# Kernel optimization log

Hardware: AMD Instinct MI355X
Metric: run time of the kernel (lower is better)

The kernel has to match this reference:

```python
import jax, jax.numpy as jnp
import numpy as np

B, S, HID = 2, 2048, 2048
H, K, D = 32, 8, 64          # query heads, kv heads, head_dim
G = H // K                   # GQA group size
ROPE_MSCALE = 1.2            # constant rope_mscale applied to q and k
SM_SCALE = 1.0 / (D ** 0.5)  # flash_attn default softmax scale


def rotate_half(x):
    h = x.shape[-1] // 2
    return jnp.concatenate([-x[..., h:], x[..., :h]], axis=-1)


def setup_inputs() -> dict:
    key = jax.random.key(0)
    k1, k2, k3, k4 = jax.random.split(key, 4)
    hidden_states = jax.random.normal(k1, (B, S, HID), dtype=jnp.float32)
    # standard rotary tables: cos/sin of shape [S, D]
    inv_freq = 1.0 / (10000.0 ** (jnp.arange(0, D, 2, dtype=jnp.float32) / D))
    freqs = jnp.outer(jnp.arange(S, dtype=jnp.float32), inv_freq)  # [S, D/2]
    emb = jnp.concatenate([freqs, freqs], axis=-1)                 # [S, D]
    cos, sin = jnp.cos(emb), jnp.sin(emb)
    per_head_scale = 1.0 + 0.1 * jax.random.normal(k2, (B, H), dtype=jnp.float32)
    Wqkv = jax.random.normal(k3, ((H + 2 * K) * D, HID), dtype=jnp.float32) * (HID ** -0.5)
    Wo = jax.random.normal(k4, (HID, H * D), dtype=jnp.float32) * ((H * D) ** -0.5)
    return {"cos": cos, "sin": sin, "hidden_states": hidden_states,
            "per_head_scale": per_head_scale, "Wqkv": Wqkv, "Wo": Wo}


def reference(cos, sin, hidden_states, per_head_scale, Wqkv, Wo):
    # fused QKV projection (CastedLinear, no bias)
    qkv = jnp.einsum('bsh,oh->bso', hidden_states, Wqkv)          # [B,S,(H+2K)*D]
    qkv = qkv.reshape(B, S, H + 2 * K, D)
    q = qkv[:, :, :H]                 # [B,S,H,D]
    k = qkv[:, :, H:H + K]            # [B,S,K,D]
    v = qkv[:, :, H + K:]             # [B,S,K,D]
    # rotary embedding: cos/sin [S,D] -> broadcast over heads via [S,1,D]
    c = cos[:, None, :]
    s_ = sin[:, None, :]
    q = q * c + rotate_half(q) * s_
    k = k * c + rotate_half(k) * s_
    # rope_mscale
    q = q * ROPE_MSCALE
    k = k * ROPE_MSCALE
    # per-head scale on queries: [B,H] -> [B,1,H,1]
    q = q * per_head_scale[:, None, :, None]
    # GQA attention without materializing repeated K/V: group query heads
    qg = q.reshape(B, S, K, G, D)
    scores = jnp.einsum('bqkgd,bskd->bkgqs', qg, k) * SM_SCALE    # [B,K,G,Sq,Sk]
    causal = jnp.arange(S)[:, None] >= jnp.arange(S)[None, :]     # [Sq,Sk]
    scores = jnp.where(causal, scores, jnp.finfo(scores.dtype).min)
    probs = jax.nn.softmax(scores, axis=-1)
    out = jnp.einsum('bkgqs,bskd->bqkgd', probs, v).reshape(B, S, H * D)
    return jnp.einsum('bso,ho->bsh', out, Wo)                     # o_proj
```

## Files before the change

### kernel.cpp

```cpp
#include <hip/hip_runtime.h>
#include <stdint.h>

typedef unsigned short u16;
typedef short short8 __attribute__((ext_vector_type(8)));
typedef float f32x4 __attribute__((ext_vector_type(4)));
typedef uint32_t u32x4 __attribute__((ext_vector_type(4)));

#define S_LEN 2048
#define NQH 32
#define NKH 8
#define DHD 64

__device__ __forceinline__ float b2f(u16 u){
  union { uint32_t i; float f; } c; c.i = ((uint32_t)u) << 16; return c.f;
}
__device__ __forceinline__ u16 f2b(float f){
  union { float f; uint32_t i; } c; c.f = f;
  uint32_t r = c.i + 0x7fffu + ((c.i >> 16) & 1u);
  return (u16)(r >> 16);
}
__device__ __forceinline__ uint32_t cvt_pk_bf16(float lo, float hi){
  uint32_t r;
  asm("v_cvt_pk_bf16_f32 %0, %1, %2" : "=v"(r) : "v"(lo), "v"(hi));
  return r;
}
__device__ __forceinline__ void gload_lds16(const void* g, void* l){
  __builtin_amdgcn_global_load_lds((const __attribute__((address_space(1))) uint32_t*)g,
                                   (__attribute__((address_space(3))) uint32_t*)l, 16, 0, 0);
}

__global__ __launch_bounds__(256) void cvt_all(const float* __restrict__ hs,
                                               const float* __restrict__ wq,
                                               const float* __restrict__ wo,
                                               u16* __restrict__ hsB,
                                               u16* __restrict__ wqB,
                                               u16* __restrict__ woB){
  int i = blockIdx.x * 256 + threadIdx.x;
  const float* src; u16* dst; int off;
  if (i < 2097152)      { src = hs; dst = hsB; off = i; }
  else if (i < 3670016) { src = wq; dst = wqB; off = i - 2097152; }
  else                  { src = wo; dst = woB; off = i - 3670016; }
  float4 v = ((const float4*)src)[off];
  uint2 o;
  o.x = (uint32_t)f2b(v.x) | ((uint32_t)f2b(v.y) << 16);
  o.y = (uint32_t)f2b(v.z) | ((uint32_t)f2b(v.w) << 16);
  ((uint2*)dst)[off] = o;
}

template<int OUT_F32>
__global__ __launch_bounds__(256)
void gemm_bt(const u16* __restrict__ A, const u16* __restrict__ Bm,
             void* __restrict__ Cp, int N, int K)
{
  __shared__ alignas(16) u16 lA[128 * 64];
  __shared__ alignas(16) u16 lB[128 * 64];
  const int tid = threadIdx.x;
  const int w = tid >> 6, l = tid & 63;
  const int lg = l >> 4, lc = l & 15;
  const int wm = w >> 1, wn = w & 1;
  const int m0 = blockIdx.y * 128, n0 = blockIdx.x * 128;
  const int srow = l >> 3, sc = l & 7;
  const size_t ldb = (size_t)K * 2;
  f32x4 acc[4][4] = {};
  const int kiters = K >> 6;
  for (int kt = 0; kt < kiters; ++kt){
    __syncthreads();
#pragma unroll
    for (int i = 0; i < 4; ++i){
      const int row = (i * 4 + w) * 8 + srow;
      const int gc = ((sc ^ (row & 7)) << 4);
      gload_lds16((const char*)A + (size_t)(m0 + row) * ldb + (size_t)kt * 128 + gc,
                  (char*)lA + row * 128 + sc * 16);
    }
#pragma unroll
    for (int i = 0; i < 4; ++i){
      const int row = (i * 4 + w) * 8 + srow;
      const int gc = ((sc ^ (row & 7)) << 4);
      gload_lds16((const char*)Bm + (size_t)(n0 + row) * ldb + (size_t)kt * 128 + gc,
                  (char*)lB + row * 128 + sc * 16);
    }
    __syncthreads();
#pragma unroll
    for (int kk = 0; kk < 2; ++kk){
      short8 af[4], bfr[4];
#pragma unroll
      for (int mi = 0; mi < 4; ++mi){
        const int row = wm * 64 + mi * 16 + lc;
        const int cc = (kk * 4 + lg) ^ (row & 7);
        af[mi] = *(const short8*)((const char*)lA + row * 128 + cc * 16);
      }
#pragma unroll
      for (int ni = 0; ni < 4; ++ni){
        const int row = wn * 64 + ni * 16 + lc;
        const int cc = (kk * 4 + lg) ^ (row & 7);
        bfr[ni] = *(const short8*)((const char*)lB + row * 128 + cc * 16);
      }
#pragma unroll
      for (int mi = 0; mi < 4; ++mi)
#pragma unroll
        for (int ni = 0; ni < 4; ++ni)
          acc[mi][ni] = __builtin_amdgcn_mfma_f32_16x16x32_bf16(af[mi], bfr[ni], acc[mi][ni], 0, 0, 0);
    }
  }
  const int r0 = m0 + wm * 64 + lg * 4;
  const int c0 = n0 + wn * 64 + lc;
#pragma unroll
  for (int mi = 0; mi < 4; ++mi)
#pragma unroll
    for (int ni = 0; ni < 4; ++ni)
#pragma unroll
      for (int j = 0; j < 4; ++j){
        const size_t idx = (size_t)(r0 + mi * 16 + j) * (size_t)N + (size_t)(c0 + ni * 16);
        if (OUT_F32) ((float*)Cp)[idx] = acc[mi][ni][j];
        else         ((u16*)Cp)[idx]  = f2b(acc[mi][ni][j]);
      }
}

__global__ __launch_bounds__(256)
void rope_kernel(const u16* __restrict__ qkv, const float* __restrict__ cosT,
                 const float* __restrict__ sinT, const float* __restrict__ phs,
                 u16* __restrict__ Qo, u16* __restrict__ Ko)
{
  int id = blockIdx.x * 256 + threadIdx.x;
  int b = (id >= 327680) ? 1 : 0;
  int rem = id - b * 327680;
  int head = rem >> 13;
  int s = (rem >> 2) & 2047;
  int d0 = (rem & 3) << 4;
  const u16* src = qkv + (((size_t)(b * S_LEN + s) * 48 + head) << 6);
  uint4 xa = *(const uint4*)(src + d0);
  uint4 xb = *(const uint4*)(src + d0 + 8);
  int d0p = (d0 + 32) & 63;
  uint4 pa = *(const uint4*)(src + d0p);
  uint4 pb = *(const uint4*)(src + d0p + 8);
  const float* cp = cosT + s * 64 + d0;
  const float* sp = sinT + s * 64 + d0;
  const float sgn = (d0 < 32) ? -1.f : 1.f;
  const float kscale = 0.18033688011112042f;
  const float scale = (head < NQH) ? 1.2f * kscale * phs[b * NQH + head] : 1.2f;
  uint32_t xs[4] = {xa.x, xa.y, xa.z, xa.w};
  uint32_t xs2[4] = {xb.x, xb.y, xb.z, xb.w};
  uint32_t ps[4] = {pa.x, pa.y, pa.z, pa.w};
  uint32_t ps2[4] = {pb.x, pb.y, pb.z, pb.w};
  uint32_t ow[8];
#pragma unroll
  for (int k = 0; k < 4; ++k){
    float v0 = b2f((u16)(xs[k] & 0xffff)) * cp[2*k]   + sgn * b2f((u16)(ps[k] & 0xffff)) * sp[2*k];
    float v1 = b2f((u16)(xs[k] >> 16))    * cp[2*k+1] + sgn * b2f((u16)(ps[k] >> 16))    * sp[2*k+1];
    ow[k] = (uint32_t)f2b(v0 * scale) | ((uint32_t)f2b(v1 * scale) << 16);
  }
#pragma unroll
  for (int k = 0; k < 4; ++k){
    float v0 = b2f((u16)(xs2[k] & 0xffff)) * cp[8+2*k]   + sgn * b2f((u16)(ps2[k] & 0xffff)) * sp[8+2*k];
    float v1 = b2f((u16)(xs2[k] >> 16))    * cp[8+2*k+1] + sgn * b2f((u16)(ps2[k] >> 16))    * sp[8+2*k+1];
    ow[4+k] = (uint32_t)f2b(v0 * scale) | ((uint32_t)f2b(v1 * scale) << 16);
  }
  u16* dst;
  if (head < NQH) dst = Qo + (((size_t)(b * NQH + head) * S_LEN + s) << 6) + d0;
  else            dst = Ko + (((size_t)(b * NKH + head - NQH) * S_LEN + s) << 6) + d0;
  uint4 o0 = {ow[0], ow[1], ow[2], ow[3]};
  uint4 o1 = {ow[4], ow[5], ow[6], ow[7]};
  *(uint4*)dst = o0;
  *(uint4*)(dst + 8) = o1;
}

__global__ __launch_bounds__(256)
void vtrans(const u16* __restrict__ qkv, u16* __restrict__ VT)
{
  int bid = blockIdx.x;
  int st = bid & 31, kh = (bid >> 5) & 7, b = bid >> 8;
  __shared__ alignas(16) u16 t[64][72];
  int tid = threadIdx.x;
  int r = tid >> 2, c4 = tid & 3;
  const u16* src = qkv + (((size_t)(b * S_LEN + st * 64 + r) * 48 + 40 + kh) << 6) + c4 * 16;
  *(uint4*)&t[r][c4 * 16]     = *(const uint4*)src;
  *(uint4*)&t[r][c4 * 16 + 8] = *(const uint4*)(src + 8);
  __syncthreads();
  u16 o[16];
#pragma unroll
  for (int i = 0; i < 16; ++i) o[i] = t[c4 * 16 + i][r];
  u16* dst = VT + ((size_t)(b * NKH + kh) * 64 + r) * S_LEN + st * 64 + c4 * 16;
  uint4 o0 = { (uint32_t)o[0] | ((uint32_t)o[1] << 16),  (uint32_t)o[2] | ((uint32_t)o[3] << 16),
               (uint32_t)o[4] | ((uint32_t)o[5] << 16),  (uint32_t)o[6] | ((uint32_t)o[7] << 16) };
  uint4 o1 = { (uint32_t)o[8] | ((uint32_t)o[9] << 16),  (uint32_t)o[10] | ((uint32_t)o[11] << 16),
               (uint32_t)o[12] | ((uint32_t)o[13] << 16),(uint32_t)o[14] | ((uint32_t)o[15] << 16) };
  *(uint4*)dst = o0;
  *(uint4*)(dst + 8) = o1;
}

__global__ __launch_bounds__(256, 2)
void attn_kernel(const u16* __restrict__ Q, const u16* __restrict__ Kr,
                 const u16* __restrict__ VT, u16* __restrict__ Ao)
{
  int bid = blockIdx.x;
  int p  = bid & 15;
  int g  = (bid >> 4) & 3;
  int kh = (bid >> 6) & 7;
  int b  = bid >> 9;
  int h = kh * 4 + g;
  const int qt0 = p, qt1 = 31 - p;

  __shared__ alignas(16) u16 lK[2][64 * 64];
  __shared__ alignas(16) u16 lV[2][64 * 64];

  const int tid = threadIdx.x;
  const int w = tid >> 6, l = tid & 63;
  const int lg = l >> 4, lc = l & 15;
  const int srow = l >> 3, sc = l & 7;

  short8 qf[2][2];
  {
    const u16* qbase = Q + ((size_t)(b * NQH + h) * S_LEN) * 64;
#pragma unroll
    for (int kk = 0; kk < 2; ++kk){
      qf[0][kk] = *(const short8*)(qbase + (size_t)(qt0 * 64 + w * 16 + lc) * 64 + kk * 32 + lg * 8);
      qf[1][kk] = *(const short8*)(qbase + (size_t)(qt1 * 64 + w * 16 + lc) * 64 + kk * 32 + lg * 8);
    }
  }

  const u16* Kb = Kr + (size_t)(b * NKH + kh) * S_LEN * 64;
  const u16* Vb = VT + (size_t)(b * NKH + kh) * 64 * S_LEN;

  f32x4 o[2][4] = {};
  float mrow[2] = {-3.0e38f, -3.0e38f};
  float lsum[2] = {0.f, 0.f};

  const int nt = qt1 + 1;

#define STAGE(T, BSEL) do { \
    _Pragma("unroll") \
    for (int i_ = 0; i_ < 2; ++i_){ \
      const int row_ = (i_ * 4 + w) * 8 + srow; \
      const int gc_ = ((sc ^ (row_ & 7)) << 4); \
      gload_lds16((const char*)(Kb + (size_t)((T) * 64 + row_) * 64) + gc_, \
                  (char*)lK[BSEL] + row_ * 128 + sc * 16); \
    } \
    _Pragma("unroll") \
    for (int i_ = 0; i_ < 2; ++i_){ \
      const int row_ = (i_ * 4 + w) * 8 + srow; \
      const int gc_ = ((sc ^ (row_ & 7)) << 4); \
      gload_lds16((const char*)(Vb + (size_t)row_ * S_LEN + (T) * 64) + gc_, \
                  (char*)lV[BSEL] + row_ * 128 + sc * 16); \
    } \
  } while (0)

  STAGE(0, 0);

  for (int t = 0; t < nt; ++t){
    const int cur = t & 1;
    const bool act0 = (t <= qt0);
    if (t + 1 < nt){
      STAGE(t + 1, cur ^ 1);
      asm volatile("s_waitcnt vmcnt(4)" ::: "memory");
    } else {
      asm volatile("s_waitcnt vmcnt(0)" ::: "memory");
    }
    __builtin_amdgcn_s_barrier();

    f32x4 sv[2][4] = {};
    __builtin_amdgcn_s_setprio(1);
#pragma unroll
    for (int kk = 0; kk < 2; ++kk){
      short8 kf[4];
#pragma unroll
      for (int nj = 0; nj < 4; ++nj){
        const int row = nj * 16 + lc;
        const int cc = (kk * 4 + lg) ^ (row & 7);
        kf[nj] = *(const short8*)((const char*)lK[cur] + row * 128 + cc * 16);
      }
      if (act0)
#pragma unroll
        for (int nj = 0; nj < 4; ++nj)
          sv[0][nj] = __builtin_amdgcn_mfma_f32_16x16x32_bf16(kf[nj], qf[0][kk], sv[0][nj], 0, 0, 0);
#pragma unroll
      for (int nj = 0; nj < 4; ++nj)
        sv[1][nj] = __builtin_amdgcn_mfma_f32_16x16x32_bf16(kf[nj], qf[1][kk], sv[1][nj], 0, 0, 0);
    }
    __builtin_amdgcn_s_setprio(0);

    uint32_t pw[2][2][4];
#pragma unroll
    for (int c = 0; c < 2; ++c){
      if (c == 0 && !act0) continue;
      const int qt = c ? qt1 : qt0;
      if (t == qt){
        const int qoff = w * 16 + lc;
#pragma unroll
        for (int nj = 0; nj < 4; ++nj)
#pragma unroll
          for (int jj = 0; jj < 4; ++jj){
            const int koff = nj * 16 + lg * 4 + jj;
            if (koff > qoff) sv[c][nj][jj] = -3.0e38f;
          }
      }
      float mu = sv[c][0][0];
#pragma unroll
      for (int nj = 0; nj < 4; ++nj)
#pragma unroll
        for (int jj = 0; jj < 4; ++jj) mu = fmaxf(mu, sv[c][nj][jj]);
      mu = fmaxf(mu, __shfl_xor(mu, 16));
      mu = fmaxf(mu, __shfl_xor(mu, 32));
      if (!__all(mu <= mrow[c] + 11.54f)){
        const float mnew = fmaxf(mrow[c], mu);
        const float sf = __builtin_amdgcn_exp2f(mrow[c] - mnew);
        mrow[c] = mnew;
        lsum[c] *= sf;
#pragma unroll
        for (int dn = 0; dn < 4; ++dn)
#pragma unroll
          for (int jj = 0; jj < 4; ++jj) o[c][dn][jj] *= sf;
      }
      const float mcur = mrow[c];
      float ps = 0.f;
#pragma unroll
      for (int nj = 0; nj < 4; ++nj)
#pragma unroll
        for (int jj = 0; jj < 4; ++jj){
          const float pv = __builtin_amdgcn_exp2f(sv[c][nj][jj] - mcur);
          sv[c][nj][jj] = pv;
          ps += pv;
        }
      ps += __shfl_xor(ps, 16);
      ps += __shfl_xor(ps, 32);
      lsum[c] += ps;
      uint32_t rx[4], ry[4];
#pragma unroll
      for (int nj = 0; nj < 4; ++nj){
        rx[nj] = cvt_pk_bf16(sv[c][nj][0], sv[c][nj][1]);
        ry[nj] = cvt_pk_bf16(sv[c][nj][2], sv[c][nj][3]);
      }
      const int srcA = (lg & 1) * 32 + lc;
      const bool hi = (lg & 2) != 0;
#pragma unroll
      for (int kk2 = 0; kk2 < 2; ++kk2){
        uint32_t x0 = (uint32_t)__shfl((int)rx[kk2 * 2],     srcA);
        uint32_t x1 = (uint32_t)__shfl((int)rx[kk2 * 2 + 1], srcA);
        uint32_t y0 = (uint32_t)__shfl((int)ry[kk2 * 2],     srcA);
        uint32_t y1 = (uint32_t)__shfl((int)ry[kk2 * 2 + 1], srcA);
        pw[c][kk2][0] = hi ? x1 : x0;
        pw[c][kk2][1] = hi ? y1 : y0;
        x0 = (uint32_t)__shfl((int)rx[kk2 * 2],     srcA + 16);
        x1 = (uint32_t)__shfl((int)rx[kk2 * 2 + 1], srcA + 16);
        y0 = (uint32_t)__shfl((int)ry[kk2 * 2],     srcA + 16);
        y1 = (uint32_t)__shfl((int)ry[kk2 * 2 + 1], srcA + 16);
        pw[c][kk2][2] = hi ? x1 : x0;
        pw[c][kk2][3] = hi ? y1 : y0;
      }
    }

    __builtin_amdgcn_s_setprio(1);
#pragma unroll
    for (int kk2 = 0; kk2 < 2; ++kk2){
      short8 vf[4];
#pragma unroll
      for (int dn = 0; dn < 4; ++dn){
        const int row = dn * 16 + lc;
        const int cc = (kk2 * 4 + lg) ^ (row & 7);
        vf[dn] = *(const short8*)((const char*)lV[cur] + row * 128 + cc * 16);
      }
#pragma unroll
      for (int c = 0; c < 2; ++c){
        if (c == 0 && !act0) continue;
        u32x4 pwv = { pw[c][kk2][0], pw[c][kk2][1], pw[c][kk2][2], pw[c][kk2][3] };
        const short8 pb = __builtin_bit_cast(short8, pwv);
#pragma unroll
        for (int dn = 0; dn < 4; ++dn)
          o[c][dn] = __builtin_amdgcn_mfma_f32_16x16x32_bf16(vf[dn], pb, o[c][dn], 0, 0, 0);
      }
    }
    __builtin_amdgcn_s_setprio(0);
    __builtin_amdgcn_s_barrier();
  }
#undef STAGE

#pragma unroll
  for (int c = 0; c < 2; ++c){
    const int qt = c ? qt1 : qt0;
    const float inv = 1.f / lsum[c];
    const int sq = qt * 64 + w * 16 + lc;
#pragma unroll
    for (int dn = 0; dn < 4; ++dn){
      uint2 pk;
      pk.x = cvt_pk_bf16(o[c][dn][0] * inv, o[c][dn][1] * inv);
      pk.y = cvt_pk_bf16(o[c][dn][2] * inv, o[c][dn][3] * inv);
      const int col = h * 64 + dn * 16 + lg * 4;
      *(uint2*)&Ao[(size_t)(b * S_LEN + sq) * 2048 + col] = pk;
    }
  }
}

extern "C" void kernel_launch(void* const* d_in, const int* in_sizes, int n_in,
                              void* d_out, int out_size, void* d_ws, size_t ws_size,
                              hipStream_t stream)
{
  const float* cosT = (const float*)d_in[0];
  const float* sinT = (const float*)d_in[1];
  const float* hs   = (const float*)d_in[2];
  const float* phs  = (const float*)d_in[3];
  const float* Wqkv = (const float*)d_in[4];
  const float* Wo   = (const float*)d_in[5];
  float* out = (float*)d_out;
  char* ws = (char*)d_ws;

  u16* hsB   = (u16*)(ws);
  u16* WqkvB = (u16*)(ws + 16777216);
  u16* WoB   = (u16*)(ws + 29360128);
  u16* qkvB  = (u16*)(ws + 37748736);
  u16* Qb    = (u16*)(ws + 62914560);
  u16* Kb    = (u16*)(ws + 79691776);
  u16* VTb   = (u16*)(ws + 83886080);
  u16* Ao    = hsB;

  cvt_all<<<18432, 256, 0, stream>>>(hs, Wqkv, Wo, hsB, WqkvB, WoB);
  gemm_bt<0><<<dim3(24, 32), 256, 0, stream>>>(hsB, WqkvB, (void*)qkvB, 3072, 2048);
  rope_kernel<<<2560, 256, 0, stream>>>(qkvB, cosT, sinT, phs, Qb, Kb);
  vtrans<<<512, 256, 0, stream>>>(qkvB, VTb);
  attn_kernel<<<1024, 256, 0, stream>>>(Qb, Kb, VTb, Ao);
  gemm_bt<1><<<dim3(16, 32), 256, 0, stream>>>(Ao, WoB, (void*)out, 2048, 2048);
}
```

Before: 248.1 us.

## Widen attention KV tile to 128 keys and defer row-sum reduction

The attention loop now stages 128-key K/V tiles per iteration instead of 64, halving the number of barrier-separated iterations and doubling the MFMA work between syncs. The V tile layout and swizzle are widened to 16 chunks, and causal masking is adapted to the 128-key diagonal tile. The per-iteration cross-lane shuffle for the softmax row sum is removed and done once at the end, since per-lane partial sums can be combined after the loop. This costs twice the LDS, which may limit occupancy, more registers for the larger score tile, and wasted work on masked halves of diagonal tiles.

```diff
diff --git a/kernel.cpp b/kernel.cpp
--- a/kernel.cpp
+++ b/kernel.cpp
@@ -200,13 +200,12 @@
   int h = kh * 4 + g;
   const int qt0 = p, qt1 = 31 - p;
 
-  __shared__ alignas(16) u16 lK[2][64 * 64];
-  __shared__ alignas(16) u16 lV[2][64 * 64];
+  __shared__ alignas(16) u16 lK[2][128 * 64];
+  __shared__ alignas(16) u16 lV[2][64 * 128];
 
   const int tid = threadIdx.x;
   const int w = tid >> 6, l = tid & 63;
   const int lg = l >> 4, lc = l & 15;
-  const int srow = l >> 3, sc = l & 7;
 
   short8 qf[2][2];
   {
@@ -225,22 +224,25 @@
   float mrow[2] = {-3.0e38f, -3.0e38f};
   float lsum[2] = {0.f, 0.f};
 
-  const int nt = qt1 + 1;
+  const int nt = (qt1 >> 1) + 1;
+  const int nt0 = qt0 >> 1;
 
 #define STAGE(T, BSEL) do { \
     _Pragma("unroll") \
-    for (int i_ = 0; i_ < 2; ++i_){ \
-      const int row_ = (i_ * 4 + w) * 8 + srow; \
-      const int gc_ = ((sc ^ (row_ & 7)) << 4); \
-      gload_lds16((const char*)(Kb + (size_t)((T) * 64 + row_) * 64) + gc_, \
-                  (char*)lK[BSEL] + row_ * 128 + sc * 16); \
+    for (int i_ = 0; i_ < 4; ++i_){ \
+      const int row_ = i_ * 32 + (tid >> 3); \
+      const int ch_  = tid & 7; \
+      const int gc_  = ((ch_ ^ (row_ & 7)) << 4); \
+      gload_lds16((const char*)(Kb + (size_t)((T) * 128 + row_) * 64) + gc_, \
+                  (char*)lK[BSEL] + row_ * 128 + ch_ * 16); \
     } \
     _Pragma("unroll") \
-    for (int i_ = 0; i_ < 2; ++i_){ \
-      const int row_ = (i_ * 4 + w) * 8 + srow; \
-      const int gc_ = ((sc ^ (row_ & 7)) << 4); \
-      gload_lds16((const char*)(Vb + (size_t)row_ * S_LEN + (T) * 64) + gc_, \
-                  (char*)lV[BSEL] + row_ * 128 + sc * 16); \
+    for (int i_ = 0; i_ < 4; ++i_){ \
+      const int row_ = i_ * 16 + (tid >> 4); \
+      const int ch_  = tid & 15; \
+      const int gc_  = ((ch_ ^ (row_ & 15)) << 4); \
+      gload_lds16((const char*)(Vb + (size_t)row_ * S_LEN + (T) * 128) + gc_, \
+                  (char*)lV[BSEL] + row_ * 256 + ch_ * 16); \
     } \
   } while (0)
 
@@ -248,54 +250,54 @@
 
   for (int t = 0; t < nt; ++t){
     const int cur = t & 1;
-    const bool act0 = (t <= qt0);
+    const bool act0 = (t <= nt0);
     if (t + 1 < nt){
       STAGE(t + 1, cur ^ 1);
-      asm volatile("s_waitcnt vmcnt(4)" ::: "memory");
+      asm volatile("s_waitcnt vmcnt(8)" ::: "memory");
     } else {
       asm volatile("s_waitcnt vmcnt(0)" ::: "memory");
     }
     __builtin_amdgcn_s_barrier();
 
-    f32x4 sv[2][4] = {};
+    f32x4 sv[2][8] = {};
     __builtin_amdgcn_s_setprio(1);
 #pragma unroll
     for (int kk = 0; kk < 2; ++kk){
-      short8 kf[4];
-#pragma unroll
-      for (int nj = 0; nj < 4; ++nj){
+      short8 kf[8];
+#pragma unroll
+      for (int nj = 0; nj < 8; ++nj){
         const int row = nj * 16 + lc;
         const int cc = (kk * 4 + lg) ^ (row & 7);
         kf[nj] = *(const short8*)((const char*)lK[cur] + row * 128 + cc * 16);
       }
       if (act0)
 #pragma unroll
-        for (int nj = 0; nj < 4; ++nj)
+        for (int nj = 0; nj < 8; ++nj)
           sv[0][nj] = __builtin_amdgcn_mfma_f32_16x16x32_bf16(kf[nj], qf[0][kk], sv[0][nj], 0, 0, 0);
 #pragma unroll
-      for (int nj = 0; nj < 4; ++nj)
+      for (int nj = 0; nj < 8; ++nj)
         sv[1][nj] = __builtin_amdgcn_mfma_f32_16x16x32_bf16(kf[nj], qf[1][kk], sv[1][nj], 0, 0, 0);
     }
     __builtin_amdgcn_s_setprio(0);
 
-    uint32_t pw[2][2][4];
+    uint32_t pw[2][4][4];
 #pragma unroll
     for (int c = 0; c < 2; ++c){
       if (c == 0 && !act0) continue;
       const int qt = c ? qt1 : qt0;
-      if (t == qt){
-        const int qoff = w * 16 + lc;
-#pragma unroll
-        for (int nj = 0; nj < 4; ++nj)
+      if (t == (qt >> 1)){
+        const int qloc = (qt & 1) * 64 + w * 16 + lc;
+#pragma unroll
+        for (int nj = 0; nj < 8; ++nj)
 #pragma unroll
           for (int jj = 0; jj < 4; ++jj){
-            const int koff = nj * 16 + lg * 4 + jj;
-            if (koff > qoff) sv[c][nj][jj] = -3.0e38f;
+            const int kloc = nj * 16 + lg * 4 + jj;
+            if (kloc > qloc) sv[c][nj][jj] = -3.0e38f;
           }
       }
       float mu = sv[c][0][0];
 #pragma unroll
-      for (int nj = 0; nj < 4; ++nj)
+      for (int nj = 0; nj < 8; ++nj)
 #pragma unroll
         for (int jj = 0; jj < 4; ++jj) mu = fmaxf(mu, sv[c][nj][jj]);
       mu = fmaxf(mu, __shfl_xor(mu, 16));
@@ -313,26 +315,24 @@
       const float mcur = mrow[c];
       float ps = 0.f;
 #pragma unroll
-      for (int nj = 0; nj < 4; ++nj)
+      for (int nj = 0; nj < 8; ++nj)
 #pragma unroll
         for (int jj = 0; jj < 4; ++jj){
           const float pv = __builtin_amdgcn_exp2f(sv[c][nj][jj] - mcur);
           sv[c][nj][jj] = pv;
           ps += pv;
         }
-      ps += __shfl_xor(ps, 16);
-      ps += __shfl_xor(ps, 32);
       lsum[c] += ps;
-      uint32_t rx[4], ry[4];
-#pragma unroll
-      for (int nj = 0; nj < 4; ++nj){
+      uint32_t rx[8], ry[8];
+#pragma unroll
+      for (int nj = 0; nj < 8; ++nj){
         rx[nj] = cvt_pk_bf16(sv[c][nj][0], sv[c][nj][1]);
         ry[nj] = cvt_pk_bf16(sv[c][nj][2], sv[c][nj][3]);
       }
       const int srcA = (lg & 1) * 32 + lc;
       const bool hi = (lg & 2) != 0;
 #pragma unroll
-      for (int kk2 = 0; kk2 < 2; ++kk2){
+      for (int kk2 = 0; kk2 < 4; ++kk2){
         uint32_t x0 = (uint32_t)__shfl((int)rx[kk2 * 2],     srcA);
         uint32_t x1 = (uint32_t)__shfl((int)rx[kk2 * 2 + 1], srcA);
         uint32_t y0 = (uint32_t)__shfl((int)ry[kk2 * 2],     srcA);
@@ -350,13 +350,13 @@
 
     __builtin_amdgcn_s_setprio(1);
 #pragma unroll
-    for (int kk2 = 0; kk2 < 2; ++kk2){
+    for (int kk2 = 0; kk2 < 4; ++kk2){
       short8 vf[4];
 #pragma unroll
       for (int dn = 0; dn < 4; ++dn){
         const int row = dn * 16 + lc;
-        const int cc = (kk2 * 4 + lg) ^ (row & 7);
-        vf[dn] = *(const short8*)((const char*)lV[cur] + row * 128 + cc * 16);
+        const int cc = (kk2 * 4 + lg) ^ (row & 15);
+        vf[dn] = *(const short8*)((const char*)lV[cur] + row * 256 + cc * 16);
       }
 #pragma unroll
       for (int c = 0; c < 2; ++c){
@@ -376,7 +376,10 @@
 #pragma unroll
   for (int c = 0; c < 2; ++c){
     const int qt = c ? qt1 : qt0;
-    const float inv = 1.f / lsum[c];
+    float ls = lsum[c];
+    ls += __shfl_xor(ls, 16);
+    ls += __shfl_xor(ls, 32);
+    const float inv = 1.f / ls;
     const int sq = qt * 64 + w * 16 + lc;
 #pragma unroll
     for (int dn = 0; dn < 4; ++dn){
```

Measured after the change: 236.2 us. 4.8% less time.
